# Kernel optimization log

Measured on AMD Instinct MI355X. Metric: run time of the kernel, lower is better.

Reference implementation:

```python
import jax, jax.numpy as jnp
import numpy as np

BITS = 8
BOUND = 2.0 ** (BITS - 1) - 1.0  # 127, symmetric int8 bound
EPS = 1e-6


def fake_quant(x, scale):
    """Symmetric fake quantization with straight-through estimator."""
    q = jnp.clip(jnp.round(x * scale), -BOUND, BOUND) / scale
    return x + jax.lax.stop_gradient(q - x)


def dense_aqt(x, w, b, mask):
    """AQT-style quantized dense: per-tensor input scale (masked stats),
    per-output-channel weight scale, int8-range fake quant, float GEMM.
    x: [N, Cin], w: [Cin, Cout], b: [Cout], mask: [N, 1]."""
    x_max = jnp.max(jnp.abs(x * mask))                       # masked per-tensor stat
    sx = BOUND / jnp.maximum(x_max, EPS)
    w_max = jnp.max(jnp.abs(w), axis=0, keepdims=True)        # [1, Cout]
    sw = BOUND / jnp.maximum(w_max, EPS)
    xq = fake_quant(x, sx)
    wq = fake_quant(w, sw)
    return jnp.matmul(xq, wq) + b


def setup_inputs() -> dict:
    key = jax.random.key(0)
    k1, k2, k3 = jax.random.split(key, 3)
    B, S, C, H = 4, 2048, 1024, 4096
    inputs = jax.random.normal(k1, (B, S, C), dtype=jnp.float32)
    padding_mask = jnp.ones((B, S, 1), dtype=jnp.float32)
    W1 = jax.random.normal(k2, (C, H), dtype=jnp.float32) * (1.0 / np.sqrt(C))
    b1 = jnp.zeros((H,), dtype=jnp.float32)
    W2 = jax.random.normal(k3, (H, C), dtype=jnp.float32) * (1.0 / np.sqrt(H))
    b2 = jnp.zeros((C,), dtype=jnp.float32)
    return {"inputs": inputs, "padding_mask": padding_mask,
            "W1": W1, "b1": b1, "W2": W2, "b2": b2}


def reference(inputs, padding_mask, W1, b1, W2, b2):
    B, S, C = inputs.shape
    x = inputs.reshape(B * S, C)
    m = padding_mask.reshape(B * S, 1)
    h = jax.nn.relu(dense_aqt(x, W1, b1, m))   # dropout is no-op (deterministic)
    out = dense_aqt(h, W2, b2, m)              # dropout is no-op (deterministic)
    return out.reshape(B, S, C)
```

## Files before the change

### kernel.cpp

```cpp
#include <hip/hip_runtime.h>
#include <hip/hip_fp16.h>
#include <stdint.h>


#define EPSQ 1e-6f
typedef int v4i __attribute__((ext_vector_type(4)));
typedef int v16i __attribute__((ext_vector_type(16)));

__device__ __forceinline__ void async16(const int8_t* g, int8_t* l) {
  __builtin_amdgcn_global_load_lds(
      (const __attribute__((address_space(1))) void*)g,
      (__attribute__((address_space(3))) void*)l, 16, 0, 0);
}
__device__ __forceinline__ unsigned short f2h(float f) {
  __half h = __float2half(f);
  return *(unsigned short*)&h;
}
__device__ __forceinline__ float4 max4(float4 m, float4 v) {
  m.x = fmaxf(m.x, fabsf(v.x)); m.y = fmaxf(m.y, fabsf(v.y));
  m.z = fmaxf(m.z, fabsf(v.z)); m.w = fmaxf(m.w, fabsf(v.w));
  return m;
}
__device__ __forceinline__ unsigned qmb(float x, float s) {
  return __float_as_uint(fmaf(x, s, 12582912.0f)) & 0xffu;
}
__device__ __forceinline__ unsigned q4f(float4 f, float s) {
  return qmb(f.x, s) | (qmb(f.y, s) << 8) | (qmb(f.z, s) << 16) |
         (__float_as_uint(fmaf(f.w, s, 12582912.0f)) << 24);
}
__device__ __forceinline__ unsigned q4h(unsigned ua, unsigned ub,
                                        __half2 s2, __half2 m2) {
  __half2 ha = __hfma2(*(__half2*)&ua, s2, m2);
  __half2 hb = __hfma2(*(__half2*)&ub, s2, m2);
  unsigned va = *(unsigned*)&ha, vb = *(unsigned*)&hb;
#if __has_builtin(__builtin_amdgcn_perm)
  return __builtin_amdgcn_perm(vb, va, 0x06040200u);
#else
  return (va & 0xffu) | ((va >> 8) & 0xff00u) |
         ((vb & 0xffu) << 16) | (((vb >> 8) & 0xff00u) << 16);
#endif
}
__device__ __forceinline__ int swzh(int b) {
  return b ^ (((b >> 10) & 1) << 5) ^ (((b >> 7) & 1) << 6);
}

__global__ __launch_bounds__(256) void k_stats(
    const float* __restrict__ x, const float* __restrict__ mask,
    const float* __restrict__ W1, const float* __restrict__ W2,
    float* __restrict__ pmaxX, float* __restrict__ pcm1, float* __restrict__ pcm2) {
  const int bx = blockIdx.x, tid = threadIdx.x;
  if (bx < 64) {
    const int sp = bx & 15, cg = bx >> 4;
    const int col = cg * 1024 + tid * 4;
    float4 m = {0.f, 0.f, 0.f, 0.f};
#pragma unroll 8
    for (int r = 0; r < 64; ++r)
      m = max4(m, *(const float4*)(W1 + (size_t)(sp * 64 + r) * 4096 + col));
    *(float4*)(pcm1 + sp * 4096 + col) = m;
  } else if (bx < 128) {
    const int sp = bx - 64;
    const int col = tid * 4;
    float4 m = {0.f, 0.f, 0.f, 0.f};
#pragma unroll 8
    for (int r = 0; r < 64; ++r)
      m = max4(m, *(const float4*)(W2 + (size_t)(sp * 64 + r) * 1024 + col));
    *(float4*)(pcm2 + sp * 1024 + col) = m;
  } else {
    __shared__ float red[4];
    const int b = bx - 128;
    float lmax = 0.f;
    for (int c = b * 256 + tid; c < 1048576; c += 262144) {
      size_t idx = (size_t)c * 8;
      float mk = fabsf(mask[idx >> 10]);
      float4 m4 = {0.f, 0.f, 0.f, 0.f};
      m4 = max4(m4, *(const float4*)(x + idx));
      m4 = max4(m4, *(const float4*)(x + idx + 4));
      lmax = fmaxf(lmax, fmaxf(fmaxf(m4.x, m4.y), fmaxf(m4.z, m4.w)) * mk);
    }
    for (int s = 32; s; s >>= 1) lmax = fmaxf(lmax, __shfl_down(lmax, s));
    if ((tid & 63) == 0) red[tid >> 6] = lmax;
    __syncthreads();
    if (tid == 0)
      pmaxX[b] = fmaxf(fmaxf(red[0], red[1]), fmaxf(red[2], red[3]));
  }
}

__global__ __launch_bounds__(256) void k_quant(
    const float* __restrict__ x, const float* __restrict__ W1, const float* __restrict__ W2,
    const float* __restrict__ pmaxX, const float* __restrict__ pcm1, const float* __restrict__ pcm2,
    int8_t* __restrict__ qx, int8_t* __restrict__ qw1, int8_t* __restrict__ qw2,
    float* __restrict__ cm1, float* __restrict__ cm2, float* __restrict__ scG) {
  const int bx = blockIdx.x, tid = threadIdx.x;
  if (bx < 2048) {
    __shared__ float red[4];
    float v = fmaxf(fmaxf(pmaxX[tid], pmaxX[tid + 256]),
                    fmaxf(pmaxX[tid + 512], pmaxX[tid + 768]));
    for (int s = 32; s; s >>= 1) v = fmaxf(v, __shfl_down(v, s));
    if ((tid & 63) == 0) red[tid >> 6] = v;
    __syncthreads();
    const float xmax = fmaxf(fmaxf(red[0], red[1]), fmaxf(red[2], red[3]));
    if (bx == 0 && tid == 0) scG[0] = xmax;
    const float s = 127.0f / fmaxf(xmax, EPSQ);
    const int wave = tid >> 6, lane = tid & 63;
    const int f = bx * 4 + wave;
    const int r = (f >> 5) * 32 + (lane & 31);
    const int k = (f & 31) * 32 + (lane >> 5) * 16;
    const float4* src = (const float4*)(x + (size_t)r * 1024 + k);
    uint4 o;
    o.x = q4f(src[0], s); o.y = q4f(src[1], s);
    o.z = q4f(src[2], s); o.w = q4f(src[3], s);
    *(uint4*)(qx + (size_t)f * 1024 + lane * 16) = o;
  } else if (bx < 2304) {
    int id = (bx - 2048) * 256 + tid;
    int n4 = id & 1023, kc = id >> 10;
    const int col = n4 * 4;
    float4 cm = {0.f, 0.f, 0.f, 0.f};
#pragma unroll
    for (int sp = 0; sp < 16; ++sp) {
      float4 p = *(const float4*)(pcm1 + sp * 4096 + col);
      cm.x = fmaxf(cm.x, p.x); cm.y = fmaxf(cm.y, p.y);
      cm.z = fmaxf(cm.z, p.z); cm.w = fmaxf(cm.w, p.w);
    }
    if (kc == 0) *(float4*)(cm1 + col) = cm;
    const float s0 = 127.0f / fmaxf(cm.x, EPSQ), s1 = 127.0f / fmaxf(cm.y, EPSQ);
    const float s2 = 127.0f / fmaxf(cm.z, EPSQ), s3 = 127.0f / fmaxf(cm.w, EPSQ);
    union { int8_t p[16]; uint4 v; } u0, u1, u2, u3;
#pragma unroll
    for (int j = 0; j < 16; ++j) {
      float4 f = *(const float4*)(W1 + (size_t)(kc * 16 + j) * 4096 + col);
      u0.p[j] = (int8_t)qmb(f.x, s0); u1.p[j] = (int8_t)qmb(f.y, s1);
      u2.p[j] = (int8_t)qmb(f.z, s2); u3.p[j] = (int8_t)qmb(f.w, s3);
    }
    int8_t* base = qw1 + ((size_t)(col >> 5) * 32 + (kc >> 1)) * 1024 +
                   (kc & 1) * 512 + (col & 31) * 16;
    *(uint4*)(base) = u0.v;      *(uint4*)(base + 16) = u1.v;
    *(uint4*)(base + 32) = u2.v; *(uint4*)(base + 48) = u3.v;
  } else {
    int id = (bx - 2304) * 256 + tid;
    int n4 = id & 255, kc = id >> 8;
    const int col = n4 * 4;
    float4 cm = {0.f, 0.f, 0.f, 0.f};
#pragma unroll
    for (int sp = 0; sp < 64; ++sp) {
      float4 p = *(const float4*)(pcm2 + sp * 1024 + col);
      cm.x = fmaxf(cm.x, p.x); cm.y = fmaxf(cm.y, p.y);
      cm.z = fmaxf(cm.z, p.z); cm.w = fmaxf(cm.w, p.w);
    }
    if (kc == 0) *(float4*)(cm2 + col) = cm;
    const float s0 = 127.0f / fmaxf(cm.x, EPSQ), s1 = 127.0f / fmaxf(cm.y, EPSQ);
    const float s2 = 127.0f / fmaxf(cm.z, EPSQ), s3 = 127.0f / fmaxf(cm.w, EPSQ);
    union { int8_t p[16]; uint4 v; } u0, u1, u2, u3;
#pragma unroll
    for (int j = 0; j < 16; ++j) {
      float4 f = *(const float4*)(W2 + (size_t)(kc * 16 + j) * 1024 + col);
      u0.p[j] = (int8_t)qmb(f.x, s0); u1.p[j] = (int8_t)qmb(f.y, s1);
      u2.p[j] = (int8_t)qmb(f.z, s2); u3.p[j] = (int8_t)qmb(f.w, s3);
    }
    int8_t* base = qw2 + ((size_t)(col >> 5) * 128 + (kc >> 1)) * 1024 +
                   (kc & 1) * 512 + (col & 31) * 16;
    *(uint4*)(base) = u0.v;      *(uint4*)(base + 16) = u1.v;
    *(uint4*)(base + 32) = u2.v; *(uint4*)(base + 48) = u3.v;
  }
}

__global__ __launch_bounds__(256, 5) void gemm1(
    const int8_t* __restrict__ A, const int8_t* __restrict__ Bt,
    const float* __restrict__ sxp, const float* __restrict__ cmax,
    const float* __restrict__ bias, const float* __restrict__ mask,
    unsigned short* __restrict__ hfrag, float* __restrict__ pmaxH) {
  constexpr int KF = 2, Kf = 32;
  __shared__ __align__(16) int8_t smem[32768];
  int8_t* const lsA = smem;
  int8_t* const lsB = smem + 16384;
  const int tid = threadIdx.x;
  const int wave = tid >> 6, lane = tid & 63;
  const int m0 = blockIdx.x * 128, n0 = blockIdx.y * 128;
  const int wm = (wave & 1) * 64, wn = (wave >> 1) * 64;

  v16i acc[2][2] = {};

  const int8_t* gA[KF]; const int8_t* gB[KF];
  int8_t* dA[KF]; int8_t* dB[KF];
#pragma unroll
  for (int kc = 0; kc < KF; ++kc) {
    gA[kc] = A + ((size_t)((m0 >> 5) + wave) * Kf + kc) * 1024 + lane * 16;
    gB[kc] = Bt + ((size_t)((n0 >> 5) + wave) * Kf + kc) * 1024 + lane * 16;
    dA[kc] = lsA + (kc * 4 + wave) * 1024 + lane * 16;
    dB[kc] = lsB + (kc * 4 + wave) * 1024 + lane * 16;
  }

  const int nsteps = 1024 / (32 * KF);
#pragma unroll
  for (int kc = 0; kc < KF; ++kc) { async16(gA[kc], dA[kc]); async16(gB[kc], dB[kc]); }

  const int mI = (wave & 1) * 2, nI = (wave >> 1) * 2;

  for (int kb = 0; kb < nsteps; ++kb) {
    const int cur = kb & 1;
    const int co = cur * (KF * 4096);
    __syncthreads();
    if (kb + 1 < nsteps) {
      const size_t ko = (size_t)(kb + 1) * (KF * 1024);
      const int po = (cur ^ 1) * (KF * 4096);
#pragma unroll
      for (int kc = 0; kc < KF; ++kc) {
        async16(gA[kc] + ko, dA[kc] + po);
        async16(gB[kc] + ko, dB[kc] + po);
      }
    }
#pragma unroll
    for (int kc = 0; kc < KF; ++kc) {
      v4i af[2], bf[2];
#pragma unroll
      for (int mt = 0; mt < 2; ++mt)
        af[mt] = *(const v4i*)(lsA + co + (kc * 4 + mI + mt) * 1024 + lane * 16);
#pragma unroll
      for (int nt = 0; nt < 2; ++nt)
        bf[nt] = *(const v4i*)(lsB + co + (kc * 4 + nI + nt) * 1024 + lane * 16);
#pragma unroll
      for (int mt = 0; mt < 2; ++mt)
#pragma unroll
        for (int nt = 0; nt < 2; ++nt)
          acc[mt][nt] = __builtin_amdgcn_mfma_i32_32x32x32_i8(af[mt], bf[nt], acc[mt][nt], 0, 0, 0);
    }
  }

  const float asc = fmaxf(sxp[0], EPSQ) * (1.0f / 127.0f);
  const int cl = lane & 31;
  const int rbase = 4 * (lane >> 5);

  float bsc[2], bv[2];
#pragma unroll
  for (int nt = 0; nt < 2; ++nt) {
    int col = n0 + wn + nt * 32 + cl;
    bsc[nt] = fmaxf(cmax[col], EPSQ) * (1.0f / 127.0f) * asc;
    bv[nt] = bias[col];
  }

  const int hwb = ((cl >> 4) * 512 + (cl & 15)) * 2;
  float lmax = 0.f;
  __syncthreads();
#pragma unroll
  for (int mt = 0; mt < 2; ++mt) {
    const int rbl = (wm >> 5) + mt;
#pragma unroll
    for (int g = 0; g < 4; ++g)
#pragma unroll
      for (int r2 = 0; r2 < 4; ++r2) {
        const int rloc = g * 8 + r2 + rbase;
        const float mk = fabsf(mask[m0 + wm + mt * 32 + rloc]);
#pragma unroll
        for (int nt = 0; nt < 2; ++nt) {
          const int kbl = (wn >> 5) + nt;
          float v = (float)acc[mt][nt][g * 4 + r2] * bsc[nt] + bv[nt];
          v = fmaxf(v, 0.f);
          *(unsigned short*)(smem + swzh((rbl * 4 + kbl) * 2048 + hwb + rloc * 32)) = f2h(v);
          lmax = fmaxf(lmax, v * mk);
        }
      }
  }
  for (int s = 32; s; s >>= 1) lmax = fmaxf(lmax, __shfl_down(lmax, s));
  __syncthreads();
  const size_t gfb = (size_t)(m0 >> 5) * 128 + (n0 >> 5);
#pragma unroll
  for (int i = 0; i < 8; ++i) {
    const int o = i * 4096 + tid * 16;
    uint4 vv = *(const uint4*)(smem + swzh(o));
    const int f = o >> 11;
    *(uint4*)((int8_t*)hfrag +
              (gfb + (size_t)(f >> 2) * 128 + (f & 3)) * 2048 + (o & 2047)) = vv;
  }
  __syncthreads();
  float* redf = (float*)smem;
  if (lane == 0) redf[wave] = lmax;
  __syncthreads();
  if (tid == 0)
    pmaxH[blockIdx.x * gridDim.y + blockIdx.y] =
        fmaxf(fmaxf(redf[0], redf[1]), fmaxf(redf[2], redf[3]));
}

__global__ __launch_bounds__(512, 4) void gemm2(
    const unsigned short* __restrict__ hfrag, const int8_t* __restrict__ Bt,
    const float* __restrict__ pmaxH, const float* __restrict__ cmax,
    const float* __restrict__ bias, float* __restrict__ out) {
  constexpr int KF = 2, Kf = 128;
  __shared__ __align__(16) int8_t smem[32768];
  int8_t* const lsA = smem;
  int8_t* const lsB = smem + 16384;
  const int tid = threadIdx.x;
  const int wave = tid >> 6, lane = tid & 63;

  float* red = (float*)smem;
  float v = 0.f;
#pragma unroll
  for (int j = 0; j < 4; ++j) v = fmaxf(v, pmaxH[tid + 512 * j]);
  for (int s = 32; s; s >>= 1) v = fmaxf(v, __shfl_down(v, s));
  if (lane == 0) red[wave] = v;
  __syncthreads();
  float hmax = red[0];
#pragma unroll
  for (int j = 1; j < 8; ++j) hmax = fmaxf(hmax, red[j]);
  __syncthreads();
  const float asc = fmaxf(hmax, EPSQ) * (1.0f / 127.0f);
  const __half sh = __float2half_rn(127.0f / fmaxf(hmax, EPSQ));
  const __half2 s2 = __halves2half2(sh, sh);
  const __half mh = __float2half_rn(1536.0f);
  const __half2 m2 = __halves2half2(mh, mh);

  const int bid = blockIdx.x;
  const int xcd = bid & 7, slot = bid >> 3;
  const int m0 = ((xcd << 3) + (slot >> 3)) * 128;
  const int n0 = (slot & 7) * 128;
  const int wm = (wave & 1) * 64, wn = (wave >> 1) * 32;

  v16i acc[2] = {};

  const int skc = wave >> 2, sfr = wave & 3;
  const uint4* hA = (const uint4*)hfrag;
  const size_t aIdx = ((size_t)((m0 >> 5) + sfr) * Kf + skc) * 128 + lane * 2;
  const int8_t* gB = Bt + ((size_t)((n0 >> 5) + sfr) * Kf + skc) * 1024 + lane * 16;
  int8_t* const dA = lsA + (skc * 4 + sfr) * 1024 + lane * 16;
  int8_t* const dB = lsB + (skc * 4 + sfr) * 1024 + lane * 16;

  const int nsteps = 4096 / (32 * KF);
  const int mI = (wave & 1) * 2, nb = wave >> 1;

  uint4 rA0 = {0, 0, 0, 0}, rB0 = {0, 0, 0, 0};
  uint4 rA1 = {0, 0, 0, 0}, rB1 = {0, 0, 0, 0};

  {
    uint4 a = hA[aIdx], b = hA[aIdx + 1];
    async16(gB, dB);
    __builtin_amdgcn_sched_barrier(0);
    rA1 = hA[aIdx + (size_t)(KF * 128)];
    rB1 = hA[aIdx + (size_t)(KF * 128) + 1];
    uint4 o;
    o.x = q4h(a.x, a.y, s2, m2); o.y = q4h(a.z, a.w, s2, m2);
    o.z = q4h(b.x, b.y, s2, m2); o.w = q4h(b.z, b.w, s2, m2);
    *(uint4*)dA = o;
  }
  asm volatile("s_waitcnt lgkmcnt(0)" ::: "memory");
  asm volatile("s_waitcnt vmcnt(2)" ::: "memory");
  __builtin_amdgcn_s_barrier();
  __builtin_amdgcn_sched_barrier(0);

#pragma unroll 2
  for (int kb = 0; kb < nsteps; ++kb) {
    const int cur = kb & 1;
    const int co = cur * 8192, po = co ^ 8192;
    const bool more = (kb + 1 < nsteps);
    const bool deep = (kb + 2 < nsteps);
    if (more) {
      async16(gB + (size_t)(kb + 1) * (KF * 1024), dB + po);
      __builtin_amdgcn_sched_barrier(0);
      if (deep) {
        const size_t ai = aIdx + (size_t)(kb + 2) * (KF * 128);
        if (cur) { rA1 = hA[ai]; rB1 = hA[ai + 1]; }
        else     { rA0 = hA[ai]; rB0 = hA[ai + 1]; }
      }
    }
#pragma unroll
    for (int kc = 0; kc < KF; ++kc) {
      v4i af0 = *(const v4i*)(lsA + co + (kc * 4 + mI) * 1024 + lane * 16);
      v4i af1 = *(const v4i*)(lsA + co + (kc * 4 + mI + 1) * 1024 + lane * 16);
      v4i bf  = *(const v4i*)(lsB + co + (kc * 4 + nb) * 1024 + lane * 16);
      acc[0] = __builtin_amdgcn_mfma_i32_32x32x32_i8(af0, bf, acc[0], 0, 0, 0);
      acc[1] = __builtin_amdgcn_mfma_i32_32x32x32_i8(af1, bf, acc[1], 0, 0, 0);
    }
    if (more) {
      const uint4 pa = cur ? rA0 : rA1;
      const uint4 pb = cur ? rB0 : rB1;
      uint4 o;
      o.x = q4h(pa.x, pa.y, s2, m2); o.y = q4h(pa.z, pa.w, s2, m2);
      o.z = q4h(pb.x, pb.y, s2, m2); o.w = q4h(pb.z, pb.w, s2, m2);
      *(uint4*)(dA + po) = o;
      asm volatile("s_waitcnt lgkmcnt(0)" ::: "memory");
      if (deep) asm volatile("s_waitcnt vmcnt(2)" ::: "memory");
      else      asm volatile("s_waitcnt vmcnt(0)" ::: "memory");
      __builtin_amdgcn_s_barrier();
      __builtin_amdgcn_sched_barrier(0);
    }
  }

  const int cl = lane & 31;
  const int rbase = 4 * (lane >> 5);
  const int col = n0 + wn + cl;
  const float bsc = fmaxf(cmax[col], EPSQ) * (1.0f / 127.0f) * asc;
  const float bv = bias[col];
#pragma unroll
  for (int mt = 0; mt < 2; ++mt)
#pragma unroll
    for (int g = 0; g < 4; ++g)
#pragma unroll
      for (int r2 = 0; r2 < 4; ++r2) {
        const int row = m0 + wm + mt * 32 + g * 8 + r2 + rbase;
        out[(size_t)row * 1024 + col] = (float)acc[mt][g * 4 + r2] * bsc + bv;
      }
}

extern "C" void kernel_launch(void* const* d_in, const int* in_sizes, int n_in,
                              void* d_out, int out_size, void* d_ws, size_t ws_size,
                              hipStream_t stream) {
  const float* x  = (const float*)d_in[0];
  const float* mk = (const float*)d_in[1];
  const float* W1 = (const float*)d_in[2];
  const float* b1 = (const float*)d_in[3];
  const float* W2 = (const float*)d_in[4];
  const float* b2 = (const float*)d_in[5];
  float* out = (float*)d_out;

  float* scG   = (float*)d_ws;
  float* pmaxX = scG + 8;
  float* pmaxH = pmaxX + 1024;
  float* pcm1  = pmaxH + 2048;
  float* pcm2  = pcm1 + 65536;
  float* cm1   = pcm2 + 65536;
  float* cm2   = cm1 + 4096;
  int8_t* qx  = (int8_t*)(cm2 + 1024);
  int8_t* qw1 = qx  + (size_t)8192 * 1024;
  int8_t* qw2 = qw1 + (size_t)4096 * 1024;
  unsigned short* h = (unsigned short*)(qw2 + (size_t)1024 * 4096);

  k_stats<<<1152, 256, 0, stream>>>(x, mk, W1, W2, pmaxX, pcm1, pcm2);
  k_quant<<<2560, 256, 0, stream>>>(x, W1, W2, pmaxX, pcm1, pcm2,
                                    qx, qw1, qw2, cm1, cm2, scG);
  gemm1<<<dim3(64, 32), 256, 0, stream>>>(qx, qw1, scG, cm1, b1, mk, h, pmaxH);
  gemm2<<<512, 512, 0, stream>>>(h, qw2, pmaxH, cm2, b2, out);
}
```

Baseline: 243.4 us.

## Restructure gemm1 with 8 waves, triple-buffered LDS pipeline, and XCD-aware tile mapping

gemm1 moves from 4 to 8 waves per block, with each wave owning a 64x32 subtile. The K loop now uses a 3-stage LDS ring with two tiles in flight, explicit waitcnt and barriers, and full unrolling. Blocks are remapped so that neighbouring tiles land on the same XCD, for better L2 reuse. The epilogue drops the swizzled LDS staging and writes fp16 fragments straight to global memory as 2-byte scattered stores, which may cost store coalescing. LDS per block grows to 48KB.

```diff
diff --git a/kernel.cpp b/kernel.cpp
--- a/kernel.cpp
+++ b/kernel.cpp
@@ -39,9 +39,6 @@
   return (va & 0xffu) | ((va >> 8) & 0xff00u) |
          ((vb & 0xffu) << 16) | (((vb >> 8) & 0xff00u) << 16);
 #endif
-}
-__device__ __forceinline__ int swzh(int b) {
-  return b ^ (((b >> 10) & 1) << 5) ^ (((b >> 7) & 1) << 6);
 }
 
 __global__ __launch_bounds__(256) void k_stats(
@@ -163,120 +160,103 @@
   }
 }
 
-__global__ __launch_bounds__(256, 5) void gemm1(
+__global__ __launch_bounds__(512, 6) void gemm1(
     const int8_t* __restrict__ A, const int8_t* __restrict__ Bt,
     const float* __restrict__ sxp, const float* __restrict__ cmax,
     const float* __restrict__ bias, const float* __restrict__ mask,
     unsigned short* __restrict__ hfrag, float* __restrict__ pmaxH) {
-  constexpr int KF = 2, Kf = 32;
-  __shared__ __align__(16) int8_t smem[32768];
-  int8_t* const lsA = smem;
-  int8_t* const lsB = smem + 16384;
+  constexpr int NST = 16;
+  __shared__ __align__(16) int8_t smem[3 * 16384];
   const int tid = threadIdx.x;
   const int wave = tid >> 6, lane = tid & 63;
-  const int m0 = blockIdx.x * 128, n0 = blockIdx.y * 128;
-  const int wm = (wave & 1) * 64, wn = (wave >> 1) * 64;
-
-  v16i acc[2][2] = {};
-
-  const int8_t* gA[KF]; const int8_t* gB[KF];
-  int8_t* dA[KF]; int8_t* dB[KF];
-#pragma unroll
-  for (int kc = 0; kc < KF; ++kc) {
-    gA[kc] = A + ((size_t)((m0 >> 5) + wave) * Kf + kc) * 1024 + lane * 16;
-    gB[kc] = Bt + ((size_t)((n0 >> 5) + wave) * Kf + kc) * 1024 + lane * 16;
-    dA[kc] = lsA + (kc * 4 + wave) * 1024 + lane * 16;
-    dB[kc] = lsB + (kc * 4 + wave) * 1024 + lane * 16;
-  }
-
-  const int nsteps = 1024 / (32 * KF);
-#pragma unroll
-  for (int kc = 0; kc < KF; ++kc) { async16(gA[kc], dA[kc]); async16(gB[kc], dB[kc]); }
-
-  const int mI = (wave & 1) * 2, nI = (wave >> 1) * 2;
-
-  for (int kb = 0; kb < nsteps; ++kb) {
-    const int cur = kb & 1;
-    const int co = cur * (KF * 4096);
-    __syncthreads();
-    if (kb + 1 < nsteps) {
-      const size_t ko = (size_t)(kb + 1) * (KF * 1024);
-      const int po = (cur ^ 1) * (KF * 4096);
-#pragma unroll
-      for (int kc = 0; kc < KF; ++kc) {
-        async16(gA[kc] + ko, dA[kc] + po);
-        async16(gB[kc] + ko, dB[kc] + po);
-      }
-    }
-#pragma unroll
-    for (int kc = 0; kc < KF; ++kc) {
-      v4i af[2], bf[2];
-#pragma unroll
-      for (int mt = 0; mt < 2; ++mt)
-        af[mt] = *(const v4i*)(lsA + co + (kc * 4 + mI + mt) * 1024 + lane * 16);
-#pragma unroll
-      for (int nt = 0; nt < 2; ++nt)
-        bf[nt] = *(const v4i*)(lsB + co + (kc * 4 + nI + nt) * 1024 + lane * 16);
-#pragma unroll
-      for (int mt = 0; mt < 2; ++mt)
-#pragma unroll
-        for (int nt = 0; nt < 2; ++nt)
-          acc[mt][nt] = __builtin_amdgcn_mfma_i32_32x32x32_i8(af[mt], bf[nt], acc[mt][nt], 0, 0, 0);
+
+  const int bid = blockIdx.x;
+  const int xcd = bid & 7, sl = bid >> 3;
+  const int m0 = ((xcd & 3) * 16 + (sl & 15)) * 128;
+  const int n0 = ((xcd >> 2) * 16 + (sl >> 4)) * 128;
+  const int wm = (wave & 1) * 64, wn = (wave >> 1) * 32;
+
+  v16i acc[2] = {};
+
+  const int skc = wave >> 2, sfr = wave & 3;
+  const int8_t* gA = A  + ((size_t)((m0 >> 5) + sfr) * 32 + skc) * 1024 + lane * 16;
+  const int8_t* gB = Bt + ((size_t)((n0 >> 5) + sfr) * 32 + skc) * 1024 + lane * 16;
+  const int soff = (skc * 4 + sfr) * 1024 + lane * 16;
+
+  async16(gA, smem + soff);
+  async16(gB, smem + 8192 + soff);
+  async16(gA + 2048, smem + 16384 + soff);
+  async16(gB + 2048, smem + 16384 + 8192 + soff);
+  asm volatile("s_waitcnt vmcnt(2)" ::: "memory");
+  __builtin_amdgcn_s_barrier();
+  __builtin_amdgcn_sched_barrier(0);
+
+  const int mI = (wave & 1) * 2, nb = wave >> 1;
+#pragma unroll
+  for (int kb = 0; kb < NST; ++kb) {
+    const int co = (kb % 3) * 16384;
+    if (kb + 2 < NST) {
+      const int po = ((kb + 2) % 3) * 16384;
+      async16(gA + (kb + 2) * 2048, smem + po + soff);
+      async16(gB + (kb + 2) * 2048, smem + po + 8192 + soff);
+    }
+    __builtin_amdgcn_sched_barrier(0);
+#pragma unroll
+    for (int kc = 0; kc < 2; ++kc) {
+      v4i af0 = *(const v4i*)(smem + co + (kc * 4 + mI) * 1024 + lane * 16);
+      v4i af1 = *(const v4i*)(smem + co + (kc * 4 + mI + 1) * 1024 + lane * 16);
+      v4i bf  = *(const v4i*)(smem + co + 8192 + (kc * 4 + nb) * 1024 + lane * 16);
+      acc[0] = __builtin_amdgcn_mfma_i32_32x32x32_i8(af0, bf, acc[0], 0, 0, 0);
+      acc[1] = __builtin_amdgcn_mfma_i32_32x32x32_i8(af1, bf, acc[1], 0, 0, 0);
+    }
+    if (kb + 1 < NST) {
+      asm volatile("s_waitcnt lgkmcnt(0)" ::: "memory");
+      if (kb + 2 < NST)
+        asm volatile("s_waitcnt vmcnt(2)" ::: "memory");
+      else
+        asm volatile("s_waitcnt vmcnt(0)" ::: "memory");
+      __builtin_amdgcn_s_barrier();
+      __builtin_amdgcn_sched_barrier(0);
     }
   }
 
   const float asc = fmaxf(sxp[0], EPSQ) * (1.0f / 127.0f);
   const int cl = lane & 31;
   const int rbase = 4 * (lane >> 5);
-
-  float bsc[2], bv[2];
-#pragma unroll
-  for (int nt = 0; nt < 2; ++nt) {
-    int col = n0 + wn + nt * 32 + cl;
-    bsc[nt] = fmaxf(cmax[col], EPSQ) * (1.0f / 127.0f) * asc;
-    bv[nt] = bias[col];
-  }
-
-  const int hwb = ((cl >> 4) * 512 + (cl & 15)) * 2;
+  const int col = n0 + wn + cl;
+  const float bsc = fmaxf(cmax[col], EPSQ) * (1.0f / 127.0f) * asc;
+  const float bv = bias[col];
+  const int hwoff = (cl >> 4) * 512 + (cl & 15);
+  const size_t kblk = (size_t)(n0 + wn) >> 5;
   float lmax = 0.f;
-  __syncthreads();
 #pragma unroll
   for (int mt = 0; mt < 2; ++mt) {
-    const int rbl = (wm >> 5) + mt;
+    const size_t rowblk = (size_t)((m0 + wm + mt * 32) >> 5);
+    unsigned short* hb = hfrag + (rowblk * 128 + kblk) * 1024 + hwoff;
+    const int rowbase = m0 + wm + mt * 32;
 #pragma unroll
     for (int g = 0; g < 4; ++g)
 #pragma unroll
       for (int r2 = 0; r2 < 4; ++r2) {
         const int rloc = g * 8 + r2 + rbase;
-        const float mk = fabsf(mask[m0 + wm + mt * 32 + rloc]);
-#pragma unroll
-        for (int nt = 0; nt < 2; ++nt) {
-          const int kbl = (wn >> 5) + nt;
-          float v = (float)acc[mt][nt][g * 4 + r2] * bsc[nt] + bv[nt];
-          v = fmaxf(v, 0.f);
-          *(unsigned short*)(smem + swzh((rbl * 4 + kbl) * 2048 + hwb + rloc * 32)) = f2h(v);
-          lmax = fmaxf(lmax, v * mk);
-        }
+        const float mk = fabsf(mask[rowbase + rloc]);
+        float v = (float)acc[mt][g * 4 + r2] * bsc + bv;
+        v = fmaxf(v, 0.f);
+        hb[rloc * 16] = f2h(v);
+        lmax = fmaxf(lmax, v * mk);
       }
   }
   for (int s = 32; s; s >>= 1) lmax = fmaxf(lmax, __shfl_down(lmax, s));
-  __syncthreads();
-  const size_t gfb = (size_t)(m0 >> 5) * 128 + (n0 >> 5);
-#pragma unroll
-  for (int i = 0; i < 8; ++i) {
-    const int o = i * 4096 + tid * 16;
-    uint4 vv = *(const uint4*)(smem + swzh(o));
-    const int f = o >> 11;
-    *(uint4*)((int8_t*)hfrag +
-              (gfb + (size_t)(f >> 2) * 128 + (f & 3)) * 2048 + (o & 2047)) = vv;
-  }
   __syncthreads();
   float* redf = (float*)smem;
   if (lane == 0) redf[wave] = lmax;
   __syncthreads();
-  if (tid == 0)
-    pmaxH[blockIdx.x * gridDim.y + blockIdx.y] =
-        fmaxf(fmaxf(redf[0], redf[1]), fmaxf(redf[2], redf[3]));
+  if (tid == 0) {
+    float r = redf[0];
+#pragma unroll
+    for (int j = 1; j < 8; ++j) r = fmaxf(r, redf[j]);
+    pmaxH[bid] = r;
+  }
 }
 
 __global__ __launch_bounds__(512, 4) void gemm2(
@@ -424,6 +404,6 @@
   k_stats<<<1152, 256, 0, stream>>>(x, mk, W1, W2, pmaxX, pcm1, pcm2);
   k_quant<<<2560, 256, 0, stream>>>(x, W1, W2, pmaxX, pcm1, pcm2,
                                     qx, qw1, qw2, cm1, cm2, scG);
-  gemm1<<<dim3(64, 32), 256, 0, stream>>>(qx, qw1, scG, cm1, b1, mk, h, pmaxH);
+  gemm1<<<2048, 512, 0, stream>>>(qx, qw1, scG, cm1, b1, mk, h, pmaxH);
   gemm2<<<512, 512, 0, stream>>>(h, qw2, pmaxH, cm2, b2, out);
 }
```

Result: faster. 223.1 us (-8.3%).
